# Kernel optimization log

Measured on AMD Instinct MI355X. Metric: run time of the kernel, lower is better.

Reference implementation:

```python
import jax, jax.numpy as jnp
import numpy as np

DN = ('NCHW', 'OIHW', 'NCHW')

def conv3x3(x, w):
    return jax.lax.conv_general_dilated(x, w, (1, 1), [(1, 1), (1, 1)], dimension_numbers=DN)

def setup_inputs() -> dict:
    key = jax.random.key(0)
    ks = jax.random.split(key, 5)
    N, C, H, W = 64, 512, 16, 16
    fan = C * 3 * 3
    s = 1.0 / np.sqrt(fan)
    x = jax.random.normal(ks[0], (N, C, H, W), dtype=jnp.float32)
    Wq = jax.random.normal(ks[1], (C, C, 3, 3), dtype=jnp.float32) * s
    Wk = jax.random.normal(ks[2], (C, C, 3, 3), dtype=jnp.float32) * s
    Wv = jax.random.normal(ks[3], (C, C, 3, 3), dtype=jnp.float32) * s
    Wc = jax.random.normal(ks[4], (C, C, 3, 3), dtype=jnp.float32) * s
    gamma = jnp.ones((C,), dtype=jnp.float32)
    beta = jnp.zeros((C,), dtype=jnp.float32)
    return {"x": x, "Wq": Wq, "Wk": Wk, "Wv": Wv, "Wc": Wc, "gamma": gamma, "beta": beta}

def reference(x, Wq, Wk, Wv, Wc, gamma, beta):
    C = x.shape[1]
    q = conv3x3(x, Wq)  # [N,C,H,W]
    k = conv3x3(x, Wk)
    v = conv3x3(x, Wv)
    # att[n,m,h,w] = sum_c q[n,c,h,w] * k[m,c,h,w] / sqrt(C); softmax over m
    att = jnp.einsum('nchw,mchw->nmhw', q, k) / jnp.sqrt(jnp.float32(C))
    att = jax.nn.softmax(att, axis=1)
    # virt[n,c,h,w] = sum_m att[n,m,h,w] * v[m,c,h,w]
    virt = jnp.einsum('nmhw,mchw->nchw', att, v)
    # GroupNorm(1, C): normalize over (C,H,W) per sample, per-channel affine
    mu = jnp.mean(virt, axis=(1, 2, 3), keepdims=True)
    var = jnp.var(virt, axis=(1, 2, 3), keepdims=True)
    virt = (virt - mu) * jax.lax.rsqrt(var + 1e-5)
    virt = virt * gamma[None, :, None, None] + beta[None, :, None, None]
    virt = jax.nn.relu(virt)
    virt = conv3x3(virt, Wc)
    # Dropout is identity in eval mode
    return x + virt
```

## Files before the change

kernel.cpp:

```cpp
#include <hip/hip_runtime.h>
#include <math.h>

typedef unsigned short u16;
typedef unsigned int u32;
typedef short short8 __attribute__((ext_vector_type(8)));
typedef float f32x4 __attribute__((ext_vector_type(4)));

#define NB 64
#define CCH 512
#define HW 256

__device__ __forceinline__ u16 f2bf(float f) {
    union { float f; u32 u; } x; x.f = f;
    u32 r = x.u + 0x7fffu + ((x.u >> 16) & 1u);
    return (u16)(r >> 16);
}
__device__ __forceinline__ float bf2f(u16 b) {
    union { u32 u; float f; } x; x.u = ((u32)b) << 16;
    return x.f;
}
__device__ __forceinline__ void gload_lds16(const u16* g, u16* l) {
    __builtin_amdgcn_global_load_lds((const __attribute__((address_space(1))) u32*)g,
                                     (__attribute__((address_space(3))) u32*)l, 16, 0, 0);
}

__global__ __launch_bounds__(256) void zero_borders(u16* __restrict__ pad) {
    const int n = blockIdx.x, t = threadIdx.x;
    short8 z = (short8){0,0,0,0,0,0,0,0};
    for (int idx = t; idx < 68 * 64; idx += 256) {
        int cell = idx >> 6, ch = idx & 63;
        int hh, ww;
        if (cell < 18)      { hh = 0;          ww = cell; }
        else if (cell < 36) { hh = 17;         ww = cell - 18; }
        else if (cell < 52) { hh = cell - 35;  ww = 0; }
        else                { hh = cell - 51;  ww = 17; }
        *(short8*)(pad + ((size_t)((n * 18 + hh) * 18 + ww)) * 512 + ch * 8) = z;
    }
}

__global__ __launch_bounds__(256) void prep_x(const float* __restrict__ x, u16* __restrict__ pad) {
    __shared__ float tl[64][65];
    const int n = blockIdx.z, c0 = blockIdx.y * 64, p0 = blockIdx.x * 64;
    const int t = threadIdx.x;
    {
        const int cc = t >> 2, ps = (t & 3) * 16;
#pragma unroll
        for (int i = 0; i < 4; ++i) {
            float4 v4 = *(const float4*)(x + (((size_t)(n * 512 + c0 + cc)) << 8) + p0 + ps + i * 4);
            tl[cc][ps + i * 4 + 0] = v4.x;
            tl[cc][ps + i * 4 + 1] = v4.y;
            tl[cc][ps + i * 4 + 2] = v4.z;
            tl[cc][ps + i * 4 + 3] = v4.w;
        }
    }
    __syncthreads();
    {
        const int pp = t >> 2, cs = (t & 3) * 16;
        short8 o0, o1;
#pragma unroll
        for (int i = 0; i < 8; ++i) o0[i] = (short)f2bf(tl[cs + i][pp]);
#pragma unroll
        for (int i = 0; i < 8; ++i) o1[i] = (short)f2bf(tl[cs + 8 + i][pp]);
        const int p = p0 + pp, h = p >> 4, wcol = p & 15;
        u16* dst = pad + ((size_t)((n * 18 + h + 1) * 18 + wcol + 1)) * 512 + c0 + cs;
        *(short8*)(dst + 0) = o0;
        *(short8*)(dst + 8) = o1;
    }
}

__global__ __launch_bounds__(256) void prep_w(
    const float* __restrict__ Wq, const float* __restrict__ Wk,
    const float* __restrict__ Wv, const float* __restrict__ Wc,
    u16* __restrict__ Wt)
{
    __shared__ float lw[4608];
    const int co = blockIdx.x, sel = blockIdx.y, t = threadIdx.x;
    const float* Ws = (sel == 0) ? Wq : (sel == 1) ? Wk : (sel == 2) ? Wv : Wc;
#pragma unroll
    for (int i = 0; i < 18; ++i) lw[t + i * 256] = Ws[(size_t)co * 4608 + t + i * 256];
    __syncthreads();
    for (int tap = 0; tap < 9; ++tap)
#pragma unroll
        for (int hh = 0; hh < 2; ++hh) {
            int ci = t + hh * 256;
            Wt[(((size_t)(sel * 9 + tap)) << 18) + (co << 9) + ci] = f2bf(lw[ci * 9 + tap]);
        }
}

__global__ __launch_bounds__(256, 2) void qkv_mfma4(
    const u16* __restrict__ pad, const u16* __restrict__ Wt,
    u16* __restrict__ q, u16* __restrict__ k, u16* __restrict__ v)
{
    __shared__ short As[3][4096];
    __shared__ short Bs[3][6144];
    const int t = threadIdx.x;
    const int l = t & 63;
    const int wid = t >> 6;

    const int o = blockIdx.x;
    const int imbase = (o >> 3) * 128;
    const int cobase = (o & 7) * 192;

    const int cl = ((l & 3) - ((l >> 3) & 3)) & 3;
    int imoffA[2], woffB[3];
#pragma unroll
    for (int rr = 0; rr < 2; ++rr) {
        const int chunk = wid * 2 + rr;
        const int imrow = imbase + chunk * 16 + (l >> 2);
        const int p = imrow >> 6, n = imrow & 63;
        imoffA[rr] = ((n * 18 + (p >> 4)) * 18 + (p & 15)) * 512 + cl * 8;
    }
#pragma unroll
    for (int rr = 0; rr < 3; ++rr) {
        const int cof = cobase + (wid * 3 + rr) * 16 + (l >> 2);
        const int sel = cof >> 9, co = cof & 511;
        woffB[rr] = sel * 9 * 262144 + co * 512 + cl * 8;
    }

    const int fp = ((l >> 4) + (l >> 1)) & 3;
    const int aoff = (l & 15) * 32 + fp * 8;
    const int boff = (wid * 48 + (l & 15)) * 32 + fp * 8;

    f32x4 acc[8][3];
#pragma unroll
    for (int i = 0; i < 8; ++i)
#pragma unroll
        for (int j = 0; j < 3; ++j) acc[i][j] = (f32x4){0.f, 0.f, 0.f, 0.f};

    auto STAGE = [&](int kt, int s) {
        const int tap = kt >> 4;
        const int ashift = ((tap / 3) * 18 + (tap % 3)) * 512 + (kt & 15) * 32;
        const int bshift = tap * 262144 + (kt & 15) * 32;
#pragma unroll
        for (int rr = 0; rr < 2; ++rr)
            gload_lds16(pad + imoffA[rr] + ashift, (u16*)(&As[s][0] + (wid * 2 + rr) * 512));
#pragma unroll
        for (int rr = 0; rr < 3; ++rr)
            gload_lds16(Wt + woffB[rr] + bshift, (u16*)(&Bs[s][0] + (wid * 3 + rr) * 512));
    };

    STAGE(0, 0);
    STAGE(1, 1);

    int s0 = 0;
    short8 fa[8], fb[3];
#pragma unroll 1
    for (int kt = 0; kt < 144; ++kt) {
        const int s2 = (s0 == 0) ? 2 : s0 - 1;
        const short* Ab = &As[s0][0];
        const short* Bb = &Bs[s0][0];

        if (kt >= 143) asm volatile("s_waitcnt vmcnt(0)" ::: "memory");
        else           asm volatile("s_waitcnt vmcnt(5)" ::: "memory");
        __builtin_amdgcn_sched_barrier(0);
        __builtin_amdgcn_s_barrier();
        __builtin_amdgcn_sched_barrier(0);

#pragma unroll
        for (int j = 0; j < 3; ++j) fb[j] = *(const short8*)(Bb + boff + j * 512);
#pragma unroll
        for (int i = 0; i < 8; ++i) fa[i] = *(const short8*)(Ab + aoff + i * 512);

        if (kt < 142) STAGE(kt + 2, s2);

        __builtin_amdgcn_s_setprio(1);
#pragma unroll
        for (int i = 0; i < 8; ++i)
#pragma unroll
            for (int j = 0; j < 3; ++j)
                acc[i][j] = __builtin_amdgcn_mfma_f32_16x16x32_bf16(fa[i], fb[j], acc[i][j], 0, 0, 0);
        __builtin_amdgcn_s_setprio(0);

        s0 = (s0 == 2) ? 0 : s0 + 1;
    }

#pragma unroll
    for (int j = 0; j < 3; ++j) {
        const int colb = cobase + wid * 48 + j * 16;
        u16* op = ((colb >> 9) == 0) ? q : (((colb >> 9) == 1) ? k : v);
        op += (colb & 511) + (l & 15);
#pragma unroll
        for (int i = 0; i < 8; ++i) {
            const int row = imbase + i * 16 + (l >> 4) * 4;
#pragma unroll
            for (int r = 0; r < 4; ++r)
                op[(size_t)(row + r) * 512] = f2bf(acc[i][j][r]);
        }
    }
}

__global__ __launch_bounds__(256, 2) void cres_mfma4(
    const u16* __restrict__ pad, const u16* __restrict__ WtC,
    const float* __restrict__ xres, float* __restrict__ out)
{
    __shared__ short As[3][4096];
    __shared__ short Bs[3][4096];
    const int t = threadIdx.x;
    const int l = t & 63;
    const int wid = t >> 6;
    const int wm = wid >> 1, wn = wid & 1;

    const int o = blockIdx.x;
    const int cobase = (o & 3) * 128;
    const int imbase = (o >> 2) * 128;

    const int cl = ((l & 3) - ((l >> 3) & 3)) & 3;
    int woffA[2], imoffB[2];
#pragma unroll
    for (int rr = 0; rr < 2; ++rr) {
        const int co = cobase + (wid * 2 + rr) * 16 + (l >> 2);
        woffA[rr] = co * 512 + cl * 8;
        const int imrow = imbase + (wid * 2 + rr) * 16 + (l >> 2);
        const int n = imrow >> 8, p = imrow & 255;
        imoffB[rr] = ((n * 18 + (p >> 4)) * 18 + (p & 15)) * 512 + cl * 8;
    }

    const int fp = ((l >> 4) + (l >> 1)) & 3;
    const int aoff = (wm * 64 + (l & 15)) * 32 + fp * 8;
    const int boff = (wn * 64 + (l & 15)) * 32 + fp * 8;

    f32x4 acc[4][4];
#pragma unroll
    for (int i = 0; i < 4; ++i)
#pragma unroll
        for (int j = 0; j < 4; ++j) acc[i][j] = (f32x4){0.f, 0.f, 0.f, 0.f};

    auto STAGE = [&](int kt, int s) {
        const int tap = kt >> 4;
        const int ashift = tap * 262144 + (kt & 15) * 32;
        const int bshift = ((tap / 3) * 18 + (tap % 3)) * 512 + (kt & 15) * 32;
#pragma unroll
        for (int rr = 0; rr < 2; ++rr) {
            gload_lds16(WtC + woffA[rr] + ashift, (u16*)(&As[s][0] + (wid * 2 + rr) * 512));
            gload_lds16(pad + imoffB[rr] + bshift, (u16*)(&Bs[s][0] + (wid * 2 + rr) * 512));
        }
    };

    STAGE(0, 0);
    STAGE(1, 1);

    int s0 = 0;
    short8 fa[4], fb[4];
#pragma unroll 1
    for (int kt = 0; kt < 144; ++kt) {
        const int s2 = (s0 == 0) ? 2 : s0 - 1;
        const short* Ab = &As[s0][0];
        const short* Bb = &Bs[s0][0];

        if (kt >= 143) asm volatile("s_waitcnt vmcnt(0)" ::: "memory");
        else           asm volatile("s_waitcnt vmcnt(4)" ::: "memory");
        __builtin_amdgcn_sched_barrier(0);
        __builtin_amdgcn_s_barrier();
        __builtin_amdgcn_sched_barrier(0);

#pragma unroll
        for (int i = 0; i < 4; ++i) fa[i] = *(const short8*)(Ab + aoff + i * 512);
#pragma unroll
        for (int j = 0; j < 4; ++j) fb[j] = *(const short8*)(Bb + boff + j * 512);

        if (kt < 142) STAGE(kt + 2, s2);

        __builtin_amdgcn_s_setprio(1);
#pragma unroll
        for (int i = 0; i < 4; ++i)
#pragma unroll
            for (int j = 0; j < 4; ++j)
                acc[i][j] = __builtin_amdgcn_mfma_f32_16x16x32_bf16(fa[i], fb[j], acc[i][j], 0, 0, 0);
        __builtin_amdgcn_s_setprio(0);

        s0 = (s0 == 2) ? 0 : s0 + 1;
    }

#pragma unroll
    for (int i = 0; i < 4; ++i)
#pragma unroll
        for (int j = 0; j < 4; ++j)
#pragma unroll
            for (int r = 0; r < 4; ++r) {
                int co = cobase + wm * 64 + i * 16 + (l >> 4) * 4 + r;
                int imrow = imbase + wn * 64 + j * 16 + (l & 15);
                int n = imrow >> 8, p = imrow & 255;
                size_t addr = (((size_t)(n * 512 + co)) << 8) + p;
                out[addr] = acc[i][j][r] + xres[addr];
            }
}

__global__ __launch_bounds__(256) void attn_kernel(
    const u16* __restrict__ qT, const u16* __restrict__ kT, u16* vvT)
{
    const int p = blockIdx.x;
    const int t = threadIdx.x;
    __shared__ float smemA[2][64][68];
    __shared__ float attb[64][68];
    const size_t pb = (size_t)p * (NB * CCH);

    const int ng = t >> 4, mg = t & 15;
    const int n0 = ng * 4, m0 = mg * 4;
    float acc[4][4];
#pragma unroll
    for (int i = 0; i < 4; ++i)
#pragma unroll
        for (int j = 0; j < 4; ++j) acc[i][j] = 0.f;

    for (int ct = 0; ct < 8; ++ct) {
        const int c0 = ct * 64;
        __syncthreads();
#pragma unroll
        for (int s = 0; s < 2; ++s) {
            int f = t + s * 256;
            int nn = f >> 3, c8 = (f & 7) * 8;
            short8 qv = *(const short8*)(qT + pb + (size_t)nn * CCH + c0 + c8);
            short8 kv = *(const short8*)(kT + pb + (size_t)nn * CCH + c0 + c8);
#pragma unroll
            for (int e = 0; e < 8; ++e) {
                smemA[0][nn][c8 + e] = bf2f((u16)qv[e]);
                smemA[1][nn][c8 + e] = bf2f((u16)kv[e]);
            }
        }
        __syncthreads();
#pragma unroll 4
        for (int c4 = 0; c4 < 16; ++c4) {
            float4 q4[4], k4[4];
#pragma unroll
            for (int i = 0; i < 4; ++i) q4[i] = *(const float4*)&smemA[0][n0 + i][c4 * 4];
#pragma unroll
            for (int j = 0; j < 4; ++j) k4[j] = *(const float4*)&smemA[1][m0 + j][c4 * 4];
#pragma unroll
            for (int i = 0; i < 4; ++i)
#pragma unroll
                for (int j = 0; j < 4; ++j) {
                    acc[i][j] = fmaf(q4[i].x, k4[j].x, acc[i][j]);
                    acc[i][j] = fmaf(q4[i].y, k4[j].y, acc[i][j]);
                    acc[i][j] = fmaf(q4[i].z, k4[j].z, acc[i][j]);
                    acc[i][j] = fmaf(q4[i].w, k4[j].w, acc[i][j]);
                }
        }
    }

    const float SCALE = 0.0441941738241592f;
#pragma unroll
    for (int i = 0; i < 4; ++i) {
        float m = fmaxf(fmaxf(acc[i][0], acc[i][1]), fmaxf(acc[i][2], acc[i][3]));
#pragma unroll
        for (int mask = 1; mask < 16; mask <<= 1) m = fmaxf(m, __shfl_xor(m, mask, 16));
        float e[4]; float s = 0.f;
#pragma unroll
        for (int j = 0; j < 4; ++j) { e[j] = __expf((acc[i][j] - m) * SCALE); s += e[j]; }
#pragma unroll
        for (int mask = 1; mask < 16; mask <<= 1) s += __shfl_xor(s, mask, 16);
        float inv = 1.f / s;
#pragma unroll
        for (int j = 0; j < 4; ++j) attb[n0 + i][m0 + j] = e[j] * inv;
    }
    __syncthreads();

    float* vs = &smemA[0][0][0];
    const int ng2 = t >> 3, cg = t & 7;
    const int nn0 = ng2 * 2, cb = cg * 16;
    for (int ct4 = 0; ct4 < 4; ++ct4) {
        const int c0 = ct4 * 128;
#pragma unroll
        for (int s = 0; s < 4; ++s) {
            int f = t + s * 256;
            int m = f >> 4, c8 = (f & 15) * 8;
            short8 vv = *(const short8*)(vvT + pb + (size_t)m * CCH + c0 + c8);
#pragma unroll
            for (int e = 0; e < 8; ++e) vs[m * 132 + c8 + e] = bf2f((u16)vv[e]);
        }
        __syncthreads();
        float acc2[2][16];
#pragma unroll
        for (int i = 0; i < 2; ++i)
#pragma unroll
            for (int j = 0; j < 16; ++j) acc2[i][j] = 0.f;
#pragma unroll 4
        for (int m = 0; m < 64; ++m) {
            float a0 = attb[nn0][m], a1 = attb[nn0 + 1][m];
#pragma unroll
            for (int k4 = 0; k4 < 4; ++k4) {
                float4 v4 = *(const float4*)&vs[m * 132 + cb + k4 * 4];
                acc2[0][k4 * 4 + 0] = fmaf(a0, v4.x, acc2[0][k4 * 4 + 0]);
                acc2[0][k4 * 4 + 1] = fmaf(a0, v4.y, acc2[0][k4 * 4 + 1]);
                acc2[0][k4 * 4 + 2] = fmaf(a0, v4.z, acc2[0][k4 * 4 + 2]);
                acc2[0][k4 * 4 + 3] = fmaf(a0, v4.w, acc2[0][k4 * 4 + 3]);
                acc2[1][k4 * 4 + 0] = fmaf(a1, v4.x, acc2[1][k4 * 4 + 0]);
                acc2[1][k4 * 4 + 1] = fmaf(a1, v4.y, acc2[1][k4 * 4 + 1]);
                acc2[1][k4 * 4 + 2] = fmaf(a1, v4.z, acc2[1][k4 * 4 + 2]);
                acc2[1][k4 * 4 + 3] = fmaf(a1, v4.w, acc2[1][k4 * 4 + 3]);
            }
        }
#pragma unroll
        for (int i = 0; i < 2; ++i)
#pragma unroll
            for (int j = 0; j < 16; ++j)
                vvT[pb + (size_t)(nn0 + i) * CCH + c0 + cb + j] = f2bf(acc2[i][j]);
        __syncthreads();
    }
}

__global__ __launch_bounds__(256) void gn_part1(
    const u16* __restrict__ virtT, float* __restrict__ partials)
{
    const int n = blockIdx.x >> 2, qr = blockIdx.x & 3, t = threadIdx.x;
    float sum = 0.f, ss = 0.f;
#pragma unroll 4
    for (int it = 0; it < 16; ++it) {
        int f = t + it * 256;
        int p = qr * 64 + (f >> 6), c = (f & 63) * 8;
        short8 vv = *(const short8*)(virtT + ((size_t)(p * 64 + n)) * 512 + c);
#pragma unroll
        for (int e = 0; e < 8; ++e) { float x = bf2f((u16)vv[e]); sum += x; ss = fmaf(x, x, ss); }
    }
#pragma unroll
    for (int off = 32; off > 0; off >>= 1) {
        sum += __shfl_down(sum, off);
        ss  += __shfl_down(ss, off);
    }
    __shared__ float rs[4], rss[4];
    const int wid = t >> 6, lane = t & 63;
    if (lane == 0) { rs[wid] = sum; rss[wid] = ss; }
    __syncthreads();
    if (t == 0) {
        partials[(n * 4 + qr) * 2 + 0] = rs[0] + rs[1] + rs[2] + rs[3];
        partials[(n * 4 + qr) * 2 + 1] = rss[0] + rss[1] + rss[2] + rss[3];
    }
}

__global__ __launch_bounds__(256) void gn_part2(
    const u16* __restrict__ virtT, const float* __restrict__ partials,
    const float* __restrict__ gamma, const float* __restrict__ beta,
    u16* __restrict__ ypad)
{
    const int n = blockIdx.x >> 2, qr = blockIdx.x & 3, t = threadIdx.x;
    __shared__ float sg[512], sb[512];
    for (int i = t; i < 512; i += 256) { sg[i] = gamma[i]; sb[i] = beta[i]; }
    float S = 0.f, SS = 0.f;
#pragma unroll
    for (int i = 0; i < 4; ++i) {
        S  += partials[(n * 4 + i) * 2 + 0];
        SS += partials[(n * 4 + i) * 2 + 1];
    }
    const float mu = S * (1.f / 131072.f);
    const float var = SS * (1.f / 131072.f) - mu * mu;
    const float rstd = rsqrtf(var + 1e-5f);
    __syncthreads();

#pragma unroll 4
    for (int it = 0; it < 16; ++it) {
        int f = t + it * 256;
        int p = qr * 64 + (f >> 6), cc = (f & 63) * 8;
        short8 vv = *(const short8*)(virtT + ((size_t)(p * 64 + n)) * 512 + cc);
        short8 ov;
#pragma unroll
        for (int e = 0; e < 8; ++e) {
            float x = (bf2f((u16)vv[e]) - mu) * rstd;
            x = fmaf(x, sg[cc + e], sb[cc + e]);
            ov[e] = (short)f2bf(fmaxf(x, 0.f));
        }
        int h = p >> 4, wcol = p & 15;
        *(short8*)(ypad + ((size_t)((n * 18 + h + 1) * 18 + wcol + 1)) * 512 + cc) = ov;
    }
}

extern "C" void kernel_launch(void* const* d_in, const int* in_sizes, int n_in,
                              void* d_out, int out_size, void* d_ws, size_t ws_size,
                              hipStream_t stream)
{
    const float* x     = (const float*)d_in[0];
    const float* Wq    = (const float*)d_in[1];
    const float* Wk    = (const float*)d_in[2];
    const float* Wv    = (const float*)d_in[3];
    const float* Wc    = (const float*)d_in[4];
    const float* gamma = (const float*)d_in[5];
    const float* beta  = (const float*)d_in[6];
    float* out = (float*)d_out;

    u16* pad = (u16*)d_ws;
    u16* Wt  = pad + 10616832;
    u16* q   = Wt + 9437184;
    u16* k   = q + 8388608;
    u16* v   = k + 8388608;
    float* gnp = (float*)k;

    zero_borders<<<dim3(64), dim3(256), 0, stream>>>(pad);
    prep_x<<<dim3(4, 8, 64), dim3(256), 0, stream>>>(x, pad);
    prep_w<<<dim3(512, 4), dim3(256), 0, stream>>>(Wq, Wk, Wv, Wc, Wt);

    qkv_mfma4<<<dim3(1024), dim3(256), 0, stream>>>(pad, Wt, q, k, v);
    attn_kernel<<<dim3(256), dim3(256), 0, stream>>>(q, k, v);
    gn_part1<<<dim3(256), dim3(256), 0, stream>>>(v, gnp);
    gn_part2<<<dim3(256), dim3(256), 0, stream>>>(v, gnp, gamma, beta, pad);
    cres_mfma4<<<dim3(512), dim3(256), 0, stream>>>(pad, Wt + 3 * 2359296, x, out);
}
```

Before: 436.6 us.

## Load QKV GEMM weight fragments directly from global into registers, bypassing LDS

```diff
diff --git a/kernel.cpp b/kernel.cpp
--- a/kernel.cpp
+++ b/kernel.cpp
@@ -87,12 +87,11 @@
         }
 }
 
-__global__ __launch_bounds__(256, 2) void qkv_mfma4(
+__global__ __launch_bounds__(256, 2) void qkv_bdir(
     const u16* __restrict__ pad, const u16* __restrict__ Wt,
     u16* __restrict__ q, u16* __restrict__ k, u16* __restrict__ v)
 {
     __shared__ short As[3][4096];
-    __shared__ short Bs[3][6144];
     const int t = threadIdx.x;
     const int l = t & 63;
     const int wid = t >> 6;
@@ -102,7 +101,7 @@
     const int cobase = (o & 7) * 192;
 
     const int cl = ((l & 3) - ((l >> 3) & 3)) & 3;
-    int imoffA[2], woffB[3];
+    int imoffA[2];
 #pragma unroll
     for (int rr = 0; rr < 2; ++rr) {
         const int chunk = wid * 2 + rr;
@@ -110,16 +109,18 @@
         const int p = imrow >> 6, n = imrow & 63;
         imoffA[rr] = ((n * 18 + (p >> 4)) * 18 + (p & 15)) * 512 + cl * 8;
     }
-#pragma unroll
-    for (int rr = 0; rr < 3; ++rr) {
-        const int cof = cobase + (wid * 3 + rr) * 16 + (l >> 2);
-        const int sel = cof >> 9, co = cof & 511;
-        woffB[rr] = sel * 9 * 262144 + co * 512 + cl * 8;
-    }
 
     const int fp = ((l >> 4) + (l >> 1)) & 3;
     const int aoff = (l & 15) * 32 + fp * 8;
-    const int boff = (wid * 48 + (l & 15)) * 32 + fp * 8;
+
+    size_t bgoff[3];
+#pragma unroll
+    for (int j = 0; j < 3; ++j) {
+        const int colb = cobase + wid * 48 + j * 16;
+        const int sel = colb >> 9;
+        bgoff[j] = (size_t)sel * 2359296 +
+                   (size_t)((colb & 511) + (l & 15)) * 512 + (l >> 4) * 8;
+    }
 
     f32x4 acc[8][3];
 #pragma unroll
@@ -127,52 +128,66 @@
 #pragma unroll
         for (int j = 0; j < 3; ++j) acc[i][j] = (f32x4){0.f, 0.f, 0.f, 0.f};
 
-    auto STAGE = [&](int kt, int s) {
+    auto STAGE_A = [&](int kt, int s) {
         const int tap = kt >> 4;
         const int ashift = ((tap / 3) * 18 + (tap % 3)) * 512 + (kt & 15) * 32;
-        const int bshift = tap * 262144 + (kt & 15) * 32;
 #pragma unroll
         for (int rr = 0; rr < 2; ++rr)
             gload_lds16(pad + imoffA[rr] + ashift, (u16*)(&As[s][0] + (wid * 2 + rr) * 512));
-#pragma unroll
-        for (int rr = 0; rr < 3; ++rr)
-            gload_lds16(Wt + woffB[rr] + bshift, (u16*)(&Bs[s][0] + (wid * 3 + rr) * 512));
     };
 
-    STAGE(0, 0);
-    STAGE(1, 1);
-
-    int s0 = 0;
-    short8 fa[8], fb[3];
+    short8 fbA[3], fbB[3];
+
+    STAGE_A(0, 0);
+    __builtin_amdgcn_sched_barrier(0);
+#pragma unroll
+    for (int j = 0; j < 3; ++j) fbA[j] = *(const short8*)(Wt + bgoff[j]);
+    __builtin_amdgcn_sched_barrier(0);
+    STAGE_A(1, 1);
+    __builtin_amdgcn_sched_barrier(0);
+
+    int s0 = 0, s2 = 2;
+
+#define QTILE(KT, CUR, NXT)                                                       \
+    {                                                                             \
+        if ((KT) == 143) asm volatile("s_waitcnt vmcnt(3)" ::: "memory");         \
+        else             asm volatile("s_waitcnt vmcnt(5)" ::: "memory");         \
+        __builtin_amdgcn_sched_barrier(0);                                        \
+        __builtin_amdgcn_s_barrier();                                             \
+        __builtin_amdgcn_sched_barrier(0);                                        \
+        if ((KT) < 143) {                                                         \
+            const int knn = (KT) + 1;                                             \
+            const size_t bsh = (size_t)(knn >> 4) * 262144 + (knn & 15) * 32;     \
+            _Pragma("unroll")                                                     \
+            for (int j = 0; j < 3; ++j)                                           \
+                NXT[j] = *(const short8*)(Wt + bgoff[j] + bsh);                   \
+        }                                                                         \
+        __builtin_amdgcn_sched_barrier(0);                                        \
+        if ((KT) < 142) STAGE_A((KT) + 2, s2);                                    \
+        __builtin_amdgcn_sched_barrier(0);                                        \
+        __builtin_amdgcn_s_setprio(1);                                            \
+        {                                                                         \
+            const short* Ab = &As[s0][0];                                         \
+            _Pragma("unroll")                                                     \
+            for (int f = 0; f < 8; ++f) {                                         \
+                short8 fa = *(const short8*)(Ab + aoff + f * 512);                \
+                _Pragma("unroll")                                                 \
+                for (int j = 0; j < 3; ++j)                                       \
+                    acc[f][j] = __builtin_amdgcn_mfma_f32_16x16x32_bf16(          \
+                        fa, CUR[j], acc[f][j], 0, 0, 0);                          \
+            }                                                                     \
+        }                                                                         \
+        __builtin_amdgcn_s_setprio(0);                                            \
+        s0 = (s0 == 2) ? 0 : s0 + 1;                                              \
+        s2 = (s2 == 2) ? 0 : s2 + 1;                                              \
+    }
+
 #pragma unroll 1
-    for (int kt = 0; kt < 144; ++kt) {
-        const int s2 = (s0 == 0) ? 2 : s0 - 1;
-        const short* Ab = &As[s0][0];
-        const short* Bb = &Bs[s0][0];
-
-        if (kt >= 143) asm volatile("s_waitcnt vmcnt(0)" ::: "memory");
-        else           asm volatile("s_waitcnt vmcnt(5)" ::: "memory");
-        __builtin_amdgcn_sched_barrier(0);
-        __builtin_amdgcn_s_barrier();
-        __builtin_amdgcn_sched_barrier(0);
-
-#pragma unroll
-        for (int j = 0; j < 3; ++j) fb[j] = *(const short8*)(Bb + boff + j * 512);
-#pragma unroll
-        for (int i = 0; i < 8; ++i) fa[i] = *(const short8*)(Ab + aoff + i * 512);
-
-        if (kt < 142) STAGE(kt + 2, s2);
-
-        __builtin_amdgcn_s_setprio(1);
-#pragma unroll
-        for (int i = 0; i < 8; ++i)
-#pragma unroll
-            for (int j = 0; j < 3; ++j)
-                acc[i][j] = __builtin_amdgcn_mfma_f32_16x16x32_bf16(fa[i], fb[j], acc[i][j], 0, 0, 0);
-        __builtin_amdgcn_s_setprio(0);
-
-        s0 = (s0 == 2) ? 0 : s0 + 1;
-    }
+    for (int kt = 0; kt < 144; kt += 2) {
+        QTILE(kt, fbA, fbB);
+        QTILE(kt + 1, fbB, fbA);
+    }
+#undef QTILE
 
 #pragma unroll
     for (int j = 0; j < 3; ++j) {
@@ -486,7 +501,7 @@
     prep_x<<<dim3(4, 8, 64), dim3(256), 0, stream>>>(x, pad);
     prep_w<<<dim3(512, 4), dim3(256), 0, stream>>>(Wq, Wk, Wv, Wc, Wt);
 
-    qkv_mfma4<<<dim3(1024), dim3(256), 0, stream>>>(pad, Wt, q, k, v);
+    qkv_bdir<<<dim3(1024), dim3(256), 0, stream>>>(pad, Wt, q, k, v);
     attn_kernel<<<dim3(256), dim3(256), 0, stream>>>(q, k, v);
     gn_part1<<<dim3(256), dim3(256), 0, stream>>>(v, gnp);
     gn_part2<<<dim3(256), dim3(256), 0, stream>>>(v, gnp, gamma, beta, pad);
```

Measured after the change: 499.3 us. 14.4% more time.

## Rewrite QKV conv GEMM with 32x32x16 MFMA and larger 256x192 block tiles

Applied to the files above, without the earlier changes.

```diff
diff --git a/kernel.cpp b/kernel.cpp
--- a/kernel.cpp
+++ b/kernel.cpp
@@ -5,6 +5,7 @@
 typedef unsigned int u32;
 typedef short short8 __attribute__((ext_vector_type(8)));
 typedef float f32x4 __attribute__((ext_vector_type(4)));
+typedef float f32x16 __attribute__((ext_vector_type(16)));
 
 #define NB 64
 #define CCH 512
@@ -87,45 +88,60 @@
         }
 }
 
-__global__ __launch_bounds__(256, 2) void qkv_mfma4(
+__global__ __launch_bounds__(512, 2) void qkv_mfma32(
     const u16* __restrict__ pad, const u16* __restrict__ Wt,
     u16* __restrict__ q, u16* __restrict__ k, u16* __restrict__ v)
 {
-    __shared__ short As[3][4096];
+    __shared__ short As[3][8192];
     __shared__ short Bs[3][6144];
     const int t = threadIdx.x;
     const int l = t & 63;
     const int wid = t >> 6;
+    const int wm = wid >> 1, wn = wid & 1;
 
     const int o = blockIdx.x;
-    const int imbase = (o >> 3) * 128;
-    const int cobase = (o & 7) * 192;
+    const int wg = (o & 7) * 64 + (o >> 3);
+    const int imbase = (wg >> 3) * 256;
+    const int cobase = (wg & 7) * 192;
 
     const int cl = ((l & 3) - ((l >> 3) & 3)) & 3;
-    int imoffA[2], woffB[3];
+    int imoffA[2], woffB[2];
 #pragma unroll
     for (int rr = 0; rr < 2; ++rr) {
         const int chunk = wid * 2 + rr;
         const int imrow = imbase + chunk * 16 + (l >> 2);
         const int p = imrow >> 6, n = imrow & 63;
         imoffA[rr] = ((n * 18 + (p >> 4)) * 18 + (p & 15)) * 512 + cl * 8;
-    }
-#pragma unroll
-    for (int rr = 0; rr < 3; ++rr) {
-        const int cof = cobase + (wid * 3 + rr) * 16 + (l >> 2);
+        const int cof = cobase + chunk * 16 + (l >> 2);
         const int sel = cof >> 9, co = cof & 511;
         woffB[rr] = sel * 9 * 262144 + co * 512 + cl * 8;
     }
 
-    const int fp = ((l >> 4) + (l >> 1)) & 3;
-    const int aoff = (l & 15) * 32 + fp * 8;
-    const int boff = (wid * 48 + (l & 15)) * 32 + fp * 8;
-
-    f32x4 acc[8][3];
-#pragma unroll
-    for (int i = 0; i < 8; ++i)
-#pragma unroll
-        for (int j = 0; j < 3; ++j) acc[i][j] = (f32x4){0.f, 0.f, 0.f, 0.f};
+    const int arow = wm * 64 + (l & 31);
+    int aoff[2][2], boff[2][3];
+#pragma unroll
+    for (int s = 0; s < 2; ++s) {
+#pragma unroll
+        for (int f = 0; f < 2; ++f) {
+            const int row = arow + f * 32;
+            const int phys = (s * 2 + (l >> 5) + (l >> 1)) & 3;
+            aoff[s][f] = row * 32 + phys * 8;
+        }
+#pragma unroll
+        for (int f = 0; f < 3; ++f) {
+            const int row = wn * 96 + f * 32 + (l & 31);
+            const int phys = (s * 2 + (l >> 5) + (l >> 1)) & 3;
+            boff[s][f] = row * 32 + phys * 8;
+        }
+    }
+
+    f32x16 acc[2][3];
+#pragma unroll
+    for (int i = 0; i < 2; ++i)
+#pragma unroll
+        for (int j = 0; j < 3; ++j)
+#pragma unroll
+            for (int e = 0; e < 16; ++e) acc[i][j][e] = 0.f;
 
     auto STAGE = [&](int kt, int s) {
         const int tap = kt >> 4;
@@ -134,41 +150,49 @@
 #pragma unroll
         for (int rr = 0; rr < 2; ++rr)
             gload_lds16(pad + imoffA[rr] + ashift, (u16*)(&As[s][0] + (wid * 2 + rr) * 512));
-#pragma unroll
-        for (int rr = 0; rr < 3; ++rr)
-            gload_lds16(Wt + woffB[rr] + bshift, (u16*)(&Bs[s][0] + (wid * 3 + rr) * 512));
+        if (wid < 6) {
+#pragma unroll
+            for (int rr = 0; rr < 2; ++rr)
+                gload_lds16(Wt + woffB[rr] + bshift, (u16*)(&Bs[s][0] + (wid * 2 + rr) * 512));
+        }
     };
 
     STAGE(0, 0);
     STAGE(1, 1);
 
     int s0 = 0;
-    short8 fa[8], fb[3];
 #pragma unroll 1
     for (int kt = 0; kt < 144; ++kt) {
         const int s2 = (s0 == 0) ? 2 : s0 - 1;
         const short* Ab = &As[s0][0];
         const short* Bb = &Bs[s0][0];
 
-        if (kt >= 143) asm volatile("s_waitcnt vmcnt(0)" ::: "memory");
-        else           asm volatile("s_waitcnt vmcnt(5)" ::: "memory");
+        if (kt >= 143)    asm volatile("s_waitcnt vmcnt(0)" ::: "memory");
+        else if (wid < 6) asm volatile("s_waitcnt vmcnt(4)" ::: "memory");
+        else              asm volatile("s_waitcnt vmcnt(2)" ::: "memory");
         __builtin_amdgcn_sched_barrier(0);
         __builtin_amdgcn_s_barrier();
         __builtin_amdgcn_sched_barrier(0);
 
-#pragma unroll
-        for (int j = 0; j < 3; ++j) fb[j] = *(const short8*)(Bb + boff + j * 512);
-#pragma unroll
-        for (int i = 0; i < 8; ++i) fa[i] = *(const short8*)(Ab + aoff + i * 512);
+        short8 fa[2][2], fb[2][3];
+#pragma unroll
+        for (int s = 0; s < 2; ++s) {
+#pragma unroll
+            for (int f = 0; f < 2; ++f) fa[s][f] = *(const short8*)(Ab + aoff[s][f]);
+#pragma unroll
+            for (int f = 0; f < 3; ++f) fb[s][f] = *(const short8*)(Bb + boff[s][f]);
+        }
 
         if (kt < 142) STAGE(kt + 2, s2);
 
         __builtin_amdgcn_s_setprio(1);
 #pragma unroll
-        for (int i = 0; i < 8; ++i)
-#pragma unroll
-            for (int j = 0; j < 3; ++j)
-                acc[i][j] = __builtin_amdgcn_mfma_f32_16x16x32_bf16(fa[i], fb[j], acc[i][j], 0, 0, 0);
+        for (int s = 0; s < 2; ++s)
+#pragma unroll
+            for (int i = 0; i < 2; ++i)
+#pragma unroll
+                for (int j = 0; j < 3; ++j)
+                    acc[i][j] = __builtin_amdgcn_mfma_f32_32x32x16_bf16(fa[s][i], fb[s][j], acc[i][j], 0, 0, 0);
         __builtin_amdgcn_s_setprio(0);
 
         s0 = (s0 == 2) ? 0 : s0 + 1;
@@ -176,15 +200,17 @@
 
 #pragma unroll
     for (int j = 0; j < 3; ++j) {
-        const int colb = cobase + wid * 48 + j * 16;
+        const int colb = cobase + wn * 96 + j * 32;
         u16* op = ((colb >> 9) == 0) ? q : (((colb >> 9) == 1) ? k : v);
-        op += (colb & 511) + (l & 15);
-#pragma unroll
-        for (int i = 0; i < 8; ++i) {
-            const int row = imbase + i * 16 + (l >> 4) * 4;
-#pragma unroll
-            for (int r = 0; r < 4; ++r)
-                op[(size_t)(row + r) * 512] = f2bf(acc[i][j][r]);
+        op += (colb & 511) + (l & 31);
+#pragma unroll
+        for (int i = 0; i < 2; ++i) {
+            const int rb = imbase + wm * 64 + i * 32 + 4 * (l >> 5);
+#pragma unroll
+            for (int r = 0; r < 16; ++r) {
+                const int row = rb + (r & 3) + 8 * (r >> 2);
+                op[(size_t)row * 512] = f2bf(acc[i][j][r]);
+            }
         }
     }
 }
@@ -486,7 +512,7 @@
     prep_x<<<dim3(4, 8, 64), dim3(256), 0, stream>>>(x, pad);
     prep_w<<<dim3(512, 4), dim3(256), 0, stream>>>(Wq, Wk, Wv, Wc, Wt);
 
-    qkv_mfma4<<<dim3(1024), dim3(256), 0, stream>>>(pad, Wt, q, k, v);
+    qkv_mfma32<<<dim3(512), dim3(512), 0, stream>>>(pad, Wt, q, k, v);
     attn_kernel<<<dim3(256), dim3(256), 0, stream>>>(q, k, v);
     gn_part1<<<dim3(256), dim3(256), 0, stream>>>(v, gnp);
     gn_part2<<<dim3(256), dim3(256), 0, stream>>>(v, gnp, gamma, beta, pad);
```

Result: slower. 458.8 us (+5.1%).
